# Performance work log

Hardware: AMD Instinct MI355X
Metric: run time of the kernel (lower is better)

The kernel has to match this reference:

```python
import jax, jax.numpy as jnp
import numpy as np

B, S, D = 8, 1024, 1024
N_HEAD, N_ACTIVE, D_ATTN = 16, 4, 128

def setup_inputs() -> dict:
    key = jax.random.key(0)
    ks = jax.random.split(key, 8)
    sc = 0.02
    return {
        "x": jax.random.normal(ks[0], (B, S, D), jnp.float32),
        "Wq": jax.random.normal(ks[1], (N_HEAD, D, D_ATTN), jnp.float32) * sc,
        "bq": jnp.zeros((N_HEAD, D_ATTN), jnp.float32),
        "Wk": jax.random.normal(ks[2], (N_HEAD, D, D_ATTN), jnp.float32) * sc,
        "bk": jnp.zeros((N_HEAD, D_ATTN), jnp.float32),
        "Wv": jax.random.normal(ks[3], (N_HEAD, D, D_ATTN), jnp.float32) * sc,
        "bv": jnp.zeros((N_HEAD, D_ATTN), jnp.float32),
        "Wr": jax.random.normal(ks[4], (D, N_HEAD), jnp.float32) * sc,
        "br": jnp.zeros((N_HEAD,), jnp.float32),
        "Wo": jax.random.normal(ks[5], (N_ACTIVE * D_ATTN, D), jnp.float32) * sc,
        "bo": jnp.zeros((D,), jnp.float32),
    }

def reference(x, Wq, bq, Wk, bk, Wv, bv, Wr, br, Wo, bo):
    # ---- routing: mean-pool router logits over seq, softmax over heads ----
    logits = jnp.einsum('bsd,dh->bsh', x, Wr) + br          # [B,S,H]
    dist = jax.nn.softmax(logits.mean(axis=1), axis=-1)     # [B,H]
    vals, idx = jax.lax.top_k(dist, N_ACTIVE)               # [B,A]
    # zeros + scatter of top-k probs, then softmax over ALL heads (as in source)
    sparse = jnp.zeros_like(dist).at[jnp.arange(B)[:, None], idx].set(vals)
    gates_full = jax.nn.softmax(sparse, axis=-1)            # [B,H]
    gates = jnp.take_along_axis(gates_full, idx, axis=-1)   # [B,A]
    # ---- gather active-head projection weights per batch ----
    Wq_a, Wk_a, Wv_a = Wq[idx], Wk[idx], Wv[idx]            # [B,A,D,Dk]
    bq_a, bk_a, bv_a = bq[idx], bk[idx], bv[idx]            # [B,A,Dk]
    Q = jnp.einsum('bsd,badk->bask', x, Wq_a) + bq_a[:, :, None, :]
    K = jnp.einsum('bsd,badk->bask', x, Wk_a) + bk_a[:, :, None, :]
    V = jnp.einsum('bsd,badk->bask', x, Wv_a) + bv_a[:, :, None, :]
    scale = 1.0 / jnp.sqrt(jnp.asarray(D_ATTN, x.dtype))
    scores = jax.nn.softmax(jnp.einsum('bask,batk->bast', Q, K) * scale, axis=-1)
    heads = jnp.einsum('bast,batk->bask', scores, V)        # [B,A,S,Dk]
    heads = heads * gates[:, :, None, None]                 # gate each head
    # concat active heads -> [B,S,A*Dk], output projection
    cat = heads.transpose(0, 2, 1, 3).reshape(B, S, N_ACTIVE * D_ATTN)
    return jnp.einsum('bsf,fd->bsd', cat, Wo) + bo
```

## Files before the change

kernel.cpp:

```cpp
#include <hip/hip_runtime.h>
#include <math.h>

#define NB 8
#define SQ 1024
#define DM 1024
#define NH 16
#define NA 4
#define DKH 128

#define WS_XPART 0
#define WS_IDX   524288
#define WS_GATES 524416
#define WS_XB    524800
#define WS_WQT   (WS_XB  + 16777216)
#define WS_WKT   (WS_WQT + 4194304)
#define WS_WVT   (WS_WKT + 4194304)
#define WS_WOT   (WS_WVT + 4194304)
#define WS_Q     (WS_WOT + 1048576)
#define WS_K     (WS_Q  + 8388608)
#define WS_VT    (WS_K  + 8388608)
#define WS_CAT   (WS_VT + 8388608)

typedef __attribute__((ext_vector_type(8))) short short8;
typedef __attribute__((ext_vector_type(4))) short short4v;
typedef __attribute__((ext_vector_type(4))) float f32x4;

#define MFMA16(a, b, c) __builtin_amdgcn_mfma_f32_16x16x32_bf16(a, b, c, 0, 0, 0)
#define GLL16(g, l) __builtin_amdgcn_global_load_lds( \
    (const __attribute__((address_space(1))) void*)(g), \
    (__attribute__((address_space(3))) void*)(l), 16, 0, 0)

__device__ __forceinline__ short f2bf(float f) {
  unsigned u = __float_as_uint(f);
  u += 0x7FFF + ((u >> 16) & 1);
  return (short)(u >> 16);
}

__global__ __launch_bounds__(256) void k_prep(const float* __restrict__ x,
                                              short* __restrict__ xb,
                                              float* __restrict__ xpart) {
  int b = blockIdx.x, ch = blockIdx.y;
  const float* xp = x + ((size_t)b*SQ + (size_t)ch*64)*DM;
  short* xbp = xb + ((size_t)b*SQ + (size_t)ch*64)*DM;
  int t = threadIdx.x;
  float a0 = 0.f, a1 = 0.f, a2 = 0.f, a3 = 0.f;
  #pragma unroll 4
  for (int r = 0; r < 64; r++) {
    float4 v = *(const float4*)&xp[(size_t)r*DM + t*4];
    short4v s4;
    s4[0] = f2bf(v.x); s4[1] = f2bf(v.y); s4[2] = f2bf(v.z); s4[3] = f2bf(v.w);
    *(short4v*)&xbp[(size_t)r*DM + t*4] = s4;
    a0 += v.x; a1 += v.y; a2 += v.z; a3 += v.w;
  }
  float4 o = {a0, a1, a2, a3};
  *(float4*)&xpart[((size_t)b*16 + ch)*DM + t*4] = o;
}

__device__ __forceinline__ void tc_tile(const float* __restrict__ in,
                                        short* __restrict__ outb,
                                        int R, int C, int r0, int c0,
                                        float (*t)[33]) {
  int tx = threadIdx.x, ty = threadIdx.y;
  #pragma unroll
  for (int i = 0; i < 4; i++)
    t[ty + 8*i][tx] = in[(size_t)(r0 + ty + 8*i) * C + c0 + tx];
  __syncthreads();
  #pragma unroll
  for (int i = 0; i < 4; i++)
    outb[(size_t)(c0 + ty + 8*i) * R + r0 + tx] = f2bf(t[tx][ty + 8*i]);
}

__global__ __launch_bounds__(256) void k_tw(
    const float* __restrict__ Wq, const float* __restrict__ Wk,
    const float* __restrict__ Wv, const float* __restrict__ Wo,
    short* __restrict__ Wqt, short* __restrict__ Wkt,
    short* __restrict__ Wvt, short* __restrict__ Wot) {
  __shared__ float t[32][33];
  int blk = blockIdx.x;
  if (blk < 6144) {
    int zz = blk >> 7;
    int within = blk & 127;
    int m = zz >> 4, hh = zz & 15;
    const float* in = (m == 0 ? Wq : m == 1 ? Wk : Wv) + (size_t)hh * DM * DKH;
    short* outb = (m == 0 ? Wqt : m == 1 ? Wkt : Wvt) + (size_t)hh * DM * DKH;
    int r0 = (within & 31) * 32;
    int c0 = (within >> 5) * 32;
    tc_tile(in, outb, DM, DKH, r0, c0, t);
  } else {
    int w2 = blk - 6144;
    int r0 = (w2 & 15) * 32;
    int c0 = (w2 >> 4) * 32;
    tc_tile(Wo, Wot, NA*DKH, DM, r0, c0, t);
  }
}

__global__ __launch_bounds__(256) void k_router(const float* __restrict__ xpart,
                                                const float* __restrict__ Wr,
                                                const float* __restrict__ br,
                                                int* __restrict__ idxout,
                                                float* __restrict__ gatesout) {
  __shared__ float xm[DM];
  __shared__ float red[16][17];
  __shared__ float logits[NH];
  int b = blockIdx.x;
  int t = threadIdx.x;
  #pragma unroll
  for (int i = 0; i < 4; i++) {
    int d = t + 256*i;
    float s = 0.f;
    for (int c = 0; c < 16; c++) s += xpart[((size_t)b*16 + c)*DM + d];
    xm[d] = s * (1.0f/(float)SQ);
  }
  __syncthreads();
  {
    int h = t & 15, c16 = t >> 4;
    float p = 0.f;
    #pragma unroll 8
    for (int j = 0; j < 64; j++) {
      int d = c16*64 + j;
      p += xm[d] * Wr[(size_t)d*NH + h];
    }
    red[c16][h] = p;
  }
  __syncthreads();
  if (t < NH) {
    float lg = br[t];
    #pragma unroll
    for (int c = 0; c < 16; c++) lg += red[c][t];
    logits[t] = lg;
  }
  __syncthreads();
  if (t == 0) {
    float mx = logits[0];
    for (int h = 1; h < NH; h++) mx = fmaxf(mx, logits[h]);
    float e[NH], sum = 0.f;
    for (int h = 0; h < NH; h++) { e[h] = expf(logits[h]-mx); sum += e[h]; }
    float dist[NH];
    for (int h = 0; h < NH; h++) dist[h] = e[h]/sum;
    int idx[NA]; float vals[NA]; bool used[NH];
    for (int h = 0; h < NH; h++) used[h] = false;
    for (int a = 0; a < NA; a++) {
      int best = -1; float bv = -1.f;
      for (int h = 0; h < NH; h++)
        if (!used[h] && dist[h] > bv) { bv = dist[h]; best = h; }
      used[best] = true; idx[a] = best; vals[a] = bv;
    }
    float sp[NH];
    for (int h = 0; h < NH; h++) sp[h] = 0.f;
    for (int a = 0; a < NA; a++) sp[idx[a]] = vals[a];
    float m2 = sp[0];
    for (int h = 1; h < NH; h++) m2 = fmaxf(m2, sp[h]);
    float e2[NH], s2 = 0.f;
    for (int h = 0; h < NH; h++) { e2[h] = expf(sp[h]-m2); s2 += e2[h]; }
    for (int a = 0; a < NA; a++) {
      idxout[b*NA + a]   = idx[a];
      gatesout[b*NA + a] = e2[idx[a]] / s2;
    }
  }
}

__global__ __launch_bounds__(256) void k_qkv(
    const short* __restrict__ xb, const short* __restrict__ Wqt,
    const short* __restrict__ Wkt, const short* __restrict__ Wvt,
    const float* __restrict__ bq, const float* __restrict__ bk,
    const float* __restrict__ bv, const int* __restrict__ idxb,
    short* __restrict__ Qo, short* __restrict__ Ko, short* __restrict__ Vto) {
  __shared__ __align__(16) short As[2][128*64];
  __shared__ __align__(16) short Bs[2][128*64];
  int blk = blockIdx.x;
  int b = blk & 7;
  int rest = blk >> 3;
  int a4 = rest & 3;
  int rem = rest >> 2;
  int which = rem % 3;
  int mt = rem / 3;
  int z = b*NA + a4;
  int h = idxb[z];
  const short* Wt; const float* bias;
  if (which == 0)      { Wt = Wqt; bias = bq; }
  else if (which == 1) { Wt = Wkt; bias = bk; }
  else                 { Wt = Wvt; bias = bv; }
  Wt += (size_t)h * (DKH * DM);
  bias += h * DKH;
  const short* Ag = xb + (size_t)b*SQ*DM + (size_t)mt*128*DM;
  int tid = threadIdx.x, lane = tid & 63, wid = tid >> 6;
  int wm = wid & 1, wn = wid >> 1;
  int l15 = lane & 15, quad = lane >> 4, l7 = lane & 7, lby8 = lane >> 3;
  int srow = lby8;
  int scol = ((l7 ^ lby8) * 8);
  f32x4 acc[4][4];
  #pragma unroll
  for (int i = 0; i < 4; i++)
    #pragma unroll
    for (int j = 0; j < 4; j++) acc[i][j] = (f32x4){0.f,0.f,0.f,0.f};
  #pragma unroll
  for (int i = 0; i < 4; i++) {
    int ci = wid*4 + i;
    GLL16(Ag + (size_t)(ci*8 + srow)*DM + scol, &As[0][ci*512]);
    GLL16(Wt + (size_t)(ci*8 + srow)*DM + scol, &Bs[0][ci*512]);
  }
  for (int kt = 0; kt < 16; kt++) {
    int cur = kt & 1;
    asm volatile("s_waitcnt vmcnt(0)" ::: "memory");
    __syncthreads();
    if (kt + 1 < 16) {
      #pragma unroll
      for (int i = 0; i < 4; i++) {
        int ci = wid*4 + i;
        GLL16(Ag + (size_t)(ci*8 + srow)*DM + (kt+1)*64 + scol, &As[cur^1][ci*512]);
        GLL16(Wt + (size_t)(ci*8 + srow)*DM + (kt+1)*64 + scol, &Bs[cur^1][ci*512]);
      }
    }
    #pragma unroll
    for (int ks = 0; ks < 2; ks++) {
      int kc = ks*4 + quad;
      short8 a[4], bf[4];
      #pragma unroll
      for (int mi = 0; mi < 4; mi++)
        a[mi] = *(const short8*)&As[cur][(wm*64 + mi*16 + l15)*64 + ((kc ^ l7)*8)];
      #pragma unroll
      for (int ni = 0; ni < 4; ni++)
        bf[ni] = *(const short8*)&Bs[cur][(wn*64 + ni*16 + l15)*64 + ((kc ^ l7)*8)];
      #pragma unroll
      for (int mi = 0; mi < 4; mi++)
        #pragma unroll
        for (int ni = 0; ni < 4; ni++)
          acc[mi][ni] = MFMA16(a[mi], bf[ni], acc[mi][ni]);
    }
  }
  if (which < 2) {
    short* outp = (which == 0 ? Qo : Ko) + (size_t)z*SQ*DKH;
    #pragma unroll
    for (int mi = 0; mi < 4; mi++)
      #pragma unroll
      for (int ni = 0; ni < 4; ni++) {
        int col = wn*64 + ni*16 + l15;
        float bcol = bias[col];
        #pragma unroll
        for (int r = 0; r < 4; r++) {
          int row = mt*128 + wm*64 + mi*16 + quad*4 + r;
          outp[(size_t)row*DKH + col] = f2bf(acc[mi][ni][r] + bcol);
        }
      }
  } else {
    short* outp = Vto + (size_t)z*DKH*SQ;
    #pragma unroll
    for (int mi = 0; mi < 4; mi++)
      #pragma unroll
      for (int ni = 0; ni < 4; ni++) {
        int col = wn*64 + ni*16 + l15;
        float bcol = bias[col];
        int row0 = mt*128 + wm*64 + mi*16 + quad*4;
        short4v v;
        #pragma unroll
        for (int r = 0; r < 4; r++) v[r] = f2bf(acc[mi][ni][r] + bcol);
        *(short4v*)&outp[(size_t)col*SQ + row0] = v;
      }
  }
}

__global__ __launch_bounds__(256) void k_attn(
    const short* __restrict__ Qg, const short* __restrict__ Kg,
    const short* __restrict__ Vtg, const float* __restrict__ gates,
    short* __restrict__ cat) {
  __shared__ __align__(16) short Ks[2][64*128];
  __shared__ __align__(16) short Vts[2][128*64];
  __shared__ __align__(16) short Ps[4*16*72];
  int blk = blockIdx.x;
  int slot = blk >> 3;
  int z = (blk & 7) + 8*(slot & 3);
  int qt = slot >> 2;
  int b = z >> 2, hs = z & 3;
  int tid = threadIdx.x, lane = tid & 63, wid = tid >> 6;
  int l15 = lane & 15, quad = lane >> 4, l7 = lane & 7, lby8 = lane >> 3;
  const short* Qp = Qg + ((size_t)z*SQ + (size_t)qt*64)*DKH;
  const short* Kp = Kg + (size_t)z*SQ*DKH;
  const short* Vp = Vtg + (size_t)z*DKH*SQ;
  short8 qa[4];
  #pragma unroll
  for (int ks = 0; ks < 4; ks++)
    qa[ks] = *(const short8*)&Qp[(size_t)(wid*16 + l15)*DKH + (ks*4 + quad)*8];
  #pragma unroll
  for (int i = 0; i < 4; i++) {
    int ci = wid*4 + i;
    int r = ci*4 + quad;
    int sc = ((l15 ^ (r & 15)) * 8);
    GLL16(Kp + (size_t)r*DKH + sc, &Ks[0][ci*512]);
    int rv = ci*8 + lby8;
    int scv = ((l7 ^ lby8) * 8);
    GLL16(Vp + (size_t)rv*SQ + scv, &Vts[0][ci*512]);
  }
  f32x4 O[8];
  #pragma unroll
  for (int dn = 0; dn < 8; dn++) O[dn] = (f32x4){0.f,0.f,0.f,0.f};
  float lsum[4] = {0.f, 0.f, 0.f, 0.f};
  const float scale = 0.08838834764831845f;
  for (int t = 0; t < 16; t++) {
    int cur = t & 1;
    asm volatile("s_waitcnt vmcnt(0)" ::: "memory");
    __syncthreads();
    if (t + 1 < 16) {
      #pragma unroll
      for (int i = 0; i < 4; i++) {
        int ci = wid*4 + i;
        int r = ci*4 + quad;
        int sc = ((l15 ^ (r & 15)) * 8);
        GLL16(Kp + (size_t)((t+1)*64 + r)*DKH + sc, &Ks[cur^1][ci*512]);
        int rv = ci*8 + lby8;
        int scv = ((l7 ^ lby8) * 8);
        GLL16(Vp + (size_t)rv*SQ + (t+1)*64 + scv, &Vts[cur^1][ci*512]);
      }
    }
    f32x4 s[4];
    #pragma unroll
    for (int nj = 0; nj < 4; nj++) s[nj] = (f32x4){0.f,0.f,0.f,0.f};
    #pragma unroll
    for (int ks = 0; ks < 4; ks++) {
      int kc = ks*4 + quad;
      #pragma unroll
      for (int nj = 0; nj < 4; nj++) {
        short8 bk8 = *(const short8*)&Ks[cur][(nj*16 + l15)*128 + ((kc ^ l15)*8)];
        s[nj] = MFMA16(qa[ks], bk8, s[nj]);
      }
    }
    #pragma unroll
    for (int r = 0; r < 4; r++) {
      float p0 = __expf(s[0][r]*scale);
      float p1 = __expf(s[1][r]*scale);
      float p2 = __expf(s[2][r]*scale);
      float p3 = __expf(s[3][r]*scale);
      lsum[r] += p0 + p1 + p2 + p3;
      int pbase = wid*1152 + (quad*4 + r)*72;
      Ps[pbase +  0 + l15] = f2bf(p0);
      Ps[pbase + 16 + l15] = f2bf(p1);
      Ps[pbase + 32 + l15] = f2bf(p2);
      Ps[pbase + 48 + l15] = f2bf(p3);
    }
    asm volatile("s_waitcnt lgkmcnt(0)" ::: "memory");
    #pragma unroll
    for (int ks2 = 0; ks2 < 2; ks2++) {
      int kc = ks2*4 + quad;
      short8 pa = *(const short8*)&Ps[wid*1152 + l15*72 + kc*8];
      #pragma unroll
      for (int dn = 0; dn < 8; dn++) {
        short8 bv8 = *(const short8*)&Vts[cur][(dn*16 + l15)*64 + ((kc ^ l7)*8)];
        O[dn] = MFMA16(pa, bv8, O[dn]);
      }
    }
  }
  float gate = gates[z];
  #pragma unroll
  for (int r = 0; r < 4; r++) {
    float rs = lsum[r];
    rs += __shfl_xor(rs, 1); rs += __shfl_xor(rs, 2);
    rs += __shfl_xor(rs, 4); rs += __shfl_xor(rs, 8);
    float sc2 = gate / rs;
    int row = qt*64 + wid*16 + quad*4 + r;
    short* cp = cat + ((size_t)(b*SQ + row))*(NA*DKH) + hs*DKH;
    #pragma unroll
    for (int dn = 0; dn < 8; dn++)
      cp[dn*16 + l15] = f2bf(O[dn][r] * sc2);
  }
}

__global__ __launch_bounds__(256) void k_out(
    const short* __restrict__ catb, const short* __restrict__ Wot,
    const float* __restrict__ bo, float* __restrict__ out) {
  __shared__ __align__(16) short As[2][128*64];
  __shared__ __align__(16) short Bs[2][128*64];
  int blk = blockIdx.x;
  int mt = (blk & 7) + 8*(blk >> 6);
  int nt = (blk >> 3) & 7;
  const short* Ag = catb + (size_t)mt*128*(NA*DKH);
  const short* Bg = Wot + (size_t)nt*128*(NA*DKH);
  int tid = threadIdx.x, lane = tid & 63, wid = tid >> 6;
  int wm = wid & 1, wn = wid >> 1;
  int l15 = lane & 15, quad = lane >> 4, l7 = lane & 7, lby8 = lane >> 3;
  int srow = lby8;
  int scol = ((l7 ^ lby8) * 8);
  f32x4 acc[4][4];
  #pragma unroll
  for (int i = 0; i < 4; i++)
    #pragma unroll
    for (int j = 0; j < 4; j++) acc[i][j] = (f32x4){0.f,0.f,0.f,0.f};
  #pragma unroll
  for (int i = 0; i < 4; i++) {
    int ci = wid*4 + i;
    GLL16(Ag + (size_t)(ci*8 + srow)*(NA*DKH) + scol, &As[0][ci*512]);
    GLL16(Bg + (size_t)(ci*8 + srow)*(NA*DKH) + scol, &Bs[0][ci*512]);
  }
  for (int kt = 0; kt < 8; kt++) {
    int cur = kt & 1;
    asm volatile("s_waitcnt vmcnt(0)" ::: "memory");
    __syncthreads();
    if (kt + 1 < 8) {
      #pragma unroll
      for (int i = 0; i < 4; i++) {
        int ci = wid*4 + i;
        GLL16(Ag + (size_t)(ci*8 + srow)*(NA*DKH) + (kt+1)*64 + scol, &As[cur^1][ci*512]);
        GLL16(Bg + (size_t)(ci*8 + srow)*(NA*DKH) + (kt+1)*64 + scol, &Bs[cur^1][ci*512]);
      }
    }
    #pragma unroll
    for (int ks = 0; ks < 2; ks++) {
      int kc = ks*4 + quad;
      short8 a[4], bf[4];
      #pragma unroll
      for (int mi = 0; mi < 4; mi++)
        a[mi] = *(const short8*)&As[cur][(wm*64 + mi*16 + l15)*64 + ((kc ^ l7)*8)];
      #pragma unroll
      for (int ni = 0; ni < 4; ni++)
        bf[ni] = *(const short8*)&Bs[cur][(wn*64 + ni*16 + l15)*64 + ((kc ^ l7)*8)];
      #pragma unroll
      for (int mi = 0; mi < 4; mi++)
        #pragma unroll
        for (int ni = 0; ni < 4; ni++)
          acc[mi][ni] = MFMA16(a[mi], bf[ni], acc[mi][ni]);
    }
  }
  #pragma unroll
  for (int mi = 0; mi < 4; mi++)
    #pragma unroll
    for (int ni = 0; ni < 4; ni++) {
      int col = nt*128 + wn*64 + ni*16 + l15;
      float bcol = bo[col];
      #pragma unroll
      for (int r = 0; r < 4; r++) {
        int row = mt*128 + wm*64 + mi*16 + quad*4 + r;
        out[(size_t)row*DM + col] = acc[mi][ni][r] + bcol;
      }
    }
}

extern "C" void kernel_launch(void* const* d_in, const int* in_sizes, int n_in,
                              void* d_out, int out_size, void* d_ws, size_t ws_size,
                              hipStream_t stream) {
  const float* x  = (const float*)d_in[0];
  const float* Wq = (const float*)d_in[1];
  const float* bq = (const float*)d_in[2];
  const float* Wk = (const float*)d_in[3];
  const float* bk = (const float*)d_in[4];
  const float* Wv = (const float*)d_in[5];
  const float* bv = (const float*)d_in[6];
  const float* Wr = (const float*)d_in[7];
  const float* br = (const float*)d_in[8];
  const float* Wo = (const float*)d_in[9];
  const float* bo = (const float*)d_in[10];
  char* ws = (char*)d_ws;
  float* xpart = (float*)(ws + WS_XPART);
  int*   idxb  = (int*)(ws + WS_IDX);
  float* gat   = (float*)(ws + WS_GATES);
  short* xb    = (short*)(ws + WS_XB);
  short* Wqt   = (short*)(ws + WS_WQT);
  short* Wkt   = (short*)(ws + WS_WKT);
  short* Wvt   = (short*)(ws + WS_WVT);
  short* Wot   = (short*)(ws + WS_WOT);
  short* Qb    = (short*)(ws + WS_Q);
  short* Kb    = (short*)(ws + WS_K);
  short* Vtb   = (short*)(ws + WS_VT);
  short* catb  = (short*)(ws + WS_CAT);
  float* out   = (float*)d_out;

  k_prep<<<dim3(NB,16), 256, 0, stream>>>(x, xb, xpart);
  k_router<<<NB, 256, 0, stream>>>(xpart, Wr, br, idxb, gat);
  k_tw<<<6656, dim3(32,8), 0, stream>>>(Wq, Wk, Wv, Wo, Wqt, Wkt, Wvt, Wot);
  k_qkv<<<768, 256, 0, stream>>>(xb, Wqt, Wkt, Wvt, bq, bk, bv, idxb, Qb, Kb, Vtb);
  k_attn<<<512, 256, 0, stream>>>(Qb, Kb, Vtb, gat, catb);
  k_out<<<512, 256, 0, stream>>>(catb, Wot, bo, out);
}
```

Baseline: 226.7 us.

## Fuse Q, K, V projections into one 128x384 tile per block

Each block now computes Q, K and V together for a 128-row tile of x, using 512 threads. Two waves load the shared x tile while six waves load the three weight slices, so the x tile is read once instead of three times. Grid size drops from 768 to 256 blocks, which raises LDS use (about 128KB for the double buffers) and register pressure with 24 accumulators per wave. On 256 CUs this leaves roughly one block per CU and may hurt occupancy.

After: 218.4 us. 3.6% less time.

```diff
diff --git a/kernel.cpp b/kernel.cpp
--- a/kernel.cpp
+++ b/kernel.cpp
@@ -159,103 +159,113 @@
   }
 }
 
-__global__ __launch_bounds__(256) void k_qkv(
+__global__ __launch_bounds__(512, 2) void k_qkv(
     const short* __restrict__ xb, const short* __restrict__ Wqt,
     const short* __restrict__ Wkt, const short* __restrict__ Wvt,
     const float* __restrict__ bq, const float* __restrict__ bk,
     const float* __restrict__ bv, const int* __restrict__ idxb,
     short* __restrict__ Qo, short* __restrict__ Ko, short* __restrict__ Vto) {
   __shared__ __align__(16) short As[2][128*64];
-  __shared__ __align__(16) short Bs[2][128*64];
+  __shared__ __align__(16) short Bs[2][384*64];
   int blk = blockIdx.x;
   int b = blk & 7;
   int rest = blk >> 3;
   int a4 = rest & 3;
-  int rem = rest >> 2;
-  int which = rem % 3;
-  int mt = rem / 3;
+  int mt = rest >> 2;
   int z = b*NA + a4;
   int h = idxb[z];
-  const short* Wt; const float* bias;
-  if (which == 0)      { Wt = Wqt; bias = bq; }
-  else if (which == 1) { Wt = Wkt; bias = bk; }
-  else                 { Wt = Wvt; bias = bv; }
-  Wt += (size_t)h * (DKH * DM);
-  bias += h * DKH;
   const short* Ag = xb + (size_t)b*SQ*DM + (size_t)mt*128*DM;
   int tid = threadIdx.x, lane = tid & 63, wid = tid >> 6;
   int wm = wid & 1, wn = wid >> 1;
-  int l15 = lane & 15, quad = lane >> 4, l7 = lane & 7, lby8 = lane >> 3;
-  int srow = lby8;
-  int scol = ((l7 ^ lby8) * 8);
-  f32x4 acc[4][4];
+  int l15 = lane & 15, quad = lane >> 4, l7 = lane & 7, srow = lane >> 3;
+  int scol = (l7 ^ srow) * 8;
+  const short* Wp;
+  {
+    int whichw = (wid - 2) >> 1;
+    const short* Wbase = (whichw == 0) ? Wqt : (whichw == 1) ? Wkt : Wvt;
+    Wp = Wbase + (size_t)h * (DKH * DM);
+  }
+  int brow_base = ((wid - 2) & 1) * 64;
+
+#define STAGE_QKV(KT, AS, BS) do {                                          \
+    if (wid < 2) {                                                          \
+      _Pragma("unroll")                                                     \
+      for (int i_ = 0; i_ < 8; i_++) {                                      \
+        int slot_ = wid*8 + i_;                                             \
+        GLL16(Ag + (size_t)(slot_*8 + srow)*DM + (KT)*64 + scol,            \
+              (AS) + slot_*512);                                            \
+      }                                                                     \
+    } else {                                                                \
+      _Pragma("unroll")                                                     \
+      for (int i_ = 0; i_ < 8; i_++) {                                      \
+        int bslot_ = (wid-2)*8 + i_;                                        \
+        GLL16(Wp + (size_t)(brow_base + i_*8 + srow)*DM + (KT)*64 + scol,   \
+              (BS) + bslot_*512);                                           \
+      }                                                                     \
+    }                                                                       \
+  } while (0)
+
+  f32x4 acc[4][6];
   #pragma unroll
   for (int i = 0; i < 4; i++)
     #pragma unroll
-    for (int j = 0; j < 4; j++) acc[i][j] = (f32x4){0.f,0.f,0.f,0.f};
-  #pragma unroll
-  for (int i = 0; i < 4; i++) {
-    int ci = wid*4 + i;
-    GLL16(Ag + (size_t)(ci*8 + srow)*DM + scol, &As[0][ci*512]);
-    GLL16(Wt + (size_t)(ci*8 + srow)*DM + scol, &Bs[0][ci*512]);
-  }
+    for (int j = 0; j < 6; j++) acc[i][j] = (f32x4){0.f,0.f,0.f,0.f};
+
+  STAGE_QKV(0, &As[0][0], &Bs[0][0]);
+
   for (int kt = 0; kt < 16; kt++) {
     int cur = kt & 1;
     asm volatile("s_waitcnt vmcnt(0)" ::: "memory");
     __syncthreads();
-    if (kt + 1 < 16) {
-      #pragma unroll
-      for (int i = 0; i < 4; i++) {
-        int ci = wid*4 + i;
-        GLL16(Ag + (size_t)(ci*8 + srow)*DM + (kt+1)*64 + scol, &As[cur^1][ci*512]);
-        GLL16(Wt + (size_t)(ci*8 + srow)*DM + (kt+1)*64 + scol, &Bs[cur^1][ci*512]);
-      }
-    }
+    if (kt + 1 < 16)
+      STAGE_QKV(kt + 1, &As[cur ^ 1][0], &Bs[cur ^ 1][0]);
     #pragma unroll
     for (int ks = 0; ks < 2; ks++) {
       int kc = ks*4 + quad;
-      short8 a[4], bf[4];
+      short8 a[4], bf[6];
       #pragma unroll
       for (int mi = 0; mi < 4; mi++)
         a[mi] = *(const short8*)&As[cur][(wm*64 + mi*16 + l15)*64 + ((kc ^ l7)*8)];
       #pragma unroll
-      for (int ni = 0; ni < 4; ni++)
-        bf[ni] = *(const short8*)&Bs[cur][(wn*64 + ni*16 + l15)*64 + ((kc ^ l7)*8)];
+      for (int ni = 0; ni < 6; ni++)
+        bf[ni] = *(const short8*)&Bs[cur][(wn*96 + ni*16 + l15)*64 + ((kc ^ l7)*8)];
       #pragma unroll
       for (int mi = 0; mi < 4; mi++)
         #pragma unroll
-        for (int ni = 0; ni < 4; ni++)
+        for (int ni = 0; ni < 6; ni++)
           acc[mi][ni] = MFMA16(a[mi], bf[ni], acc[mi][ni]);
     }
   }
-  if (which < 2) {
-    short* outp = (which == 0 ? Qo : Ko) + (size_t)z*SQ*DKH;
-    #pragma unroll
-    for (int mi = 0; mi < 4; mi++)
-      #pragma unroll
-      for (int ni = 0; ni < 4; ni++) {
-        int col = wn*64 + ni*16 + l15;
-        float bcol = bias[col];
+#undef STAGE_QKV
+
+  #pragma unroll
+  for (int ni = 0; ni < 6; ni++) {
+    int col = wn*96 + ni*16 + l15;
+    int whichc = (wn*96 + ni*16) >> 7;
+    int cl = col & 127;
+    const float* bp = (whichc == 0) ? bq : (whichc == 1) ? bk : bv;
+    float bcol = bp[h*DKH + cl];
+    if (whichc < 2) {
+      short* outp = ((whichc == 0) ? Qo : Ko) + (size_t)z*SQ*DKH;
+      #pragma unroll
+      for (int mi = 0; mi < 4; mi++) {
         #pragma unroll
         for (int r = 0; r < 4; r++) {
           int row = mt*128 + wm*64 + mi*16 + quad*4 + r;
-          outp[(size_t)row*DKH + col] = f2bf(acc[mi][ni][r] + bcol);
+          outp[(size_t)row*DKH + cl] = f2bf(acc[mi][ni][r] + bcol);
         }
       }
-  } else {
-    short* outp = Vto + (size_t)z*DKH*SQ;
-    #pragma unroll
-    for (int mi = 0; mi < 4; mi++)
-      #pragma unroll
-      for (int ni = 0; ni < 4; ni++) {
-        int col = wn*64 + ni*16 + l15;
-        float bcol = bias[col];
+    } else {
+      short* outp = Vto + (size_t)z*DKH*SQ;
+      #pragma unroll
+      for (int mi = 0; mi < 4; mi++) {
         int row0 = mt*128 + wm*64 + mi*16 + quad*4;
         short4v v;
         #pragma unroll
         for (int r = 0; r < 4; r++) v[r] = f2bf(acc[mi][ni][r] + bcol);
-        *(short4v*)&outp[(size_t)col*SQ + row0] = v;
-      }
+        *(short4v*)&outp[(size_t)cl*SQ + row0] = v;
+      }
+    }
   }
 }
 
@@ -464,7 +474,7 @@
   k_prep<<<dim3(NB,16), 256, 0, stream>>>(x, xb, xpart);
   k_router<<<NB, 256, 0, stream>>>(xpart, Wr, br, idxb, gat);
   k_tw<<<6656, dim3(32,8), 0, stream>>>(Wq, Wk, Wv, Wo, Wqt, Wkt, Wvt, Wot);
-  k_qkv<<<768, 256, 0, stream>>>(xb, Wqt, Wkt, Wvt, bq, bk, bv, idxb, Qb, Kb, Vtb);
+  k_qkv<<<256, 512, 0, stream>>>(xb, Wqt, Wkt, Wvt, bq, bk, bv, idxb, Qb, Kb, Vtb);
   k_attn<<<512, 256, 0, stream>>>(Qb, Kb, Vtb, gat, catb);
   k_out<<<512, 256, 0, stream>>>(catb, Wot, bo, out);
 }
```
